# Performance work log

Hardware: AMD Instinct MI355X
Metric: run time of the kernel (lower is better)

## Reference

```python
import jax, jax.numpy as jnp
import numpy as np

N = 65536      # number of points
D = 3          # spatial dimension (init arg 'dimension')
C = 64         # feature channels
K = 16         # neighbors returned by faiss knn search
BLOCK = 512    # query block size for chunked brute-force distances
GRID = 128     # spatial_size


def setup_inputs() -> dict:
    key = jax.random.key(0)
    k1, k2 = jax.random.split(key)
    coords = jax.random.randint(k1, (N, D), 0, GRID, dtype=jnp.int32)
    features = jax.random.normal(k2, (N, C), dtype=jnp.float32)
    return {"coords": coords, "features": features}


def reference(coords, features):
    """Brute-force KNN over integer point coords (faiss-equivalent exact L2
    search), then sparse input-layer construction: for each point, gather the
    features of its K nearest neighbors and sum them (SCN InputLayer mode=3)."""
    cf = coords.astype(jnp.float32)                 # [N, D]
    db_sq = jnp.sum(cf * cf, axis=1)                # [N]

    n_blocks = N // BLOCK
    queries = cf.reshape(n_blocks, BLOCK, D)

    def step(_, q):                                 # q: [BLOCK, D]
        q_sq = jnp.sum(q * q, axis=1)               # [BLOCK]
        # squared L2 distances to all database points: [BLOCK, N]
        dist = q_sq[:, None] - 2.0 * (q @ cf.T) + db_sq[None, :]
        _, idx = jax.lax.top_k(-dist, K)            # [BLOCK, K] nearest indices
        nb = features[idx]                          # irregular gather [BLOCK, K, C]
        return None, jnp.sum(nb, axis=1)            # mode=3: sum duplicates/neighbors

    _, out = jax.lax.scan(step, None, queries)      # [n_blocks, BLOCK, C]
    return out.reshape(N, C)
```

## Files before the change

kernel.cpp:

```cpp
#include <hip/hip_runtime.h>


typedef unsigned int uint;
typedef unsigned short ushort;
typedef short short2v __attribute__((ext_vector_type(2)));

#define NPTS   65536
#define NCELL  32768
#define BBLK   256
#define BTPB   256

static __device__ inline short2v u2s(uint v) { union { uint u; short2v s; } c; c.u = v; return c.s; }
static __device__ inline uint s2u(short2v v) { union { uint u; short2v s; } c; c.s = v; return c.u; }

static __device__ inline int dot2acc(short2v a, short2v b, int c) {
#if __has_builtin(__builtin_amdgcn_sdot2)
    return __builtin_amdgcn_sdot2(a, b, c, false);
#else
    return (int)a.x * (int)b.x + (int)a.y * (int)b.y + c;
#endif
}

static __device__ __forceinline__ void gridbar(uint* bar, uint target) {
    __syncthreads();
    if (threadIdx.x == 0) {
        asm volatile("s_waitcnt vmcnt(0)" ::: "memory");
        __hip_atomic_fetch_add(bar, 1u, __ATOMIC_RELAXED, __HIP_MEMORY_SCOPE_AGENT);
        while (__hip_atomic_load(bar, __ATOMIC_RELAXED, __HIP_MEMORY_SCOPE_AGENT) < target)
            __builtin_amdgcn_s_sleep(4);
    }
    __syncthreads();
}

__global__ __launch_bounds__(BTPB) void build(const int* __restrict__ coords,
                                              uint* __restrict__ bar,
                                              uint* __restrict__ counts,
                                              uint* __restrict__ starts,
                                              uint* __restrict__ cursors,
                                              uint2* __restrict__ sorted) {
    __shared__ uint wsum[4];
    __shared__ uint rsum[4];
    int b = blockIdx.x, tid = threadIdx.x;
    int i = b * BTPB + tid;
    int lane = tid & 63, wv = tid >> 6;

    int x = coords[3 * i + 0], y = coords[3 * i + 1], z = coords[3 * i + 2];
    int cell = (x >> 2) | ((y >> 2) << 5) | ((z >> 2) << 10);
    atomicAdd(&counts[cell], 1u);
    gridbar(bar, BBLK);

    uint* bsums = (uint*)sorted;
    uint c = 0, excl = 0;
    if (b < 128) {
        int t2 = b * 256 + tid;
        c = __hip_atomic_load(&counts[t2], __ATOMIC_RELAXED, __HIP_MEMORY_SCOPE_AGENT);
        uint v = c;
#pragma unroll
        for (int off = 1; off < 64; off <<= 1) {
            uint u = __shfl_up(v, off, 64);
            if (lane >= off) v += u;
        }
        if (lane == 63) wsum[wv] = v;
        __syncthreads();
        uint woff = 0, btot = 0;
#pragma unroll
        for (int j = 0; j < 4; ++j) {
            uint w = wsum[j];
            woff += (j < wv) ? w : 0u;
            btot += w;
        }
        excl = woff + v - c;
        if (tid == 0)
            __hip_atomic_store(&bsums[b], btot, __ATOMIC_RELAXED, __HIP_MEMORY_SCOPE_AGENT);
    }
    gridbar(bar, 2 * BBLK);

    if (b < 128) {
        uint s = 0;
        if (tid < 128 && tid < b)
            s = __hip_atomic_load(&bsums[tid], __ATOMIC_RELAXED, __HIP_MEMORY_SCOPE_AGENT);
#pragma unroll
        for (int off = 32; off; off >>= 1) s += __shfl_xor(s, off, 64);
        if (lane == 0) rsum[wv] = s;
        __syncthreads();
        uint blockoff = rsum[0] + rsum[1] + rsum[2] + rsum[3];
        int t2 = b * 256 + tid;
        uint st = blockoff + excl;
        starts[t2] = st;
        __hip_atomic_store(&cursors[t2], st, __ATOMIC_RELAXED, __HIP_MEMORY_SCOPE_AGENT);
        if (t2 == NCELL - 1) starts[NCELL] = st + c;
    }
    gridbar(bar, 3 * BBLK);

    uint pos = atomicAdd(&cursors[cell], 1u);
    sorted[pos] = make_uint2((uint)(x | (y << 16)), (uint)(i | (z << 16)));
}

__global__ __launch_bounds__(256, 8) void knn_search(const uint* __restrict__ starts,
                                                     const uint2* __restrict__ sorted,
                                                     const float* __restrict__ feat,
                                                     float* __restrict__ out) {
    int blk  = (blockIdx.x & 7) * 256 + (blockIdx.x >> 3);
    int wave = threadIdx.x >> 6;
    int lane = threadIdx.x & 63;
    int qslot = lane & 7;
    int slice = lane >> 3;
    int qpos = blk * 32 + wave * 8 + qslot;

    uint2 me = sorted[qpos];
    uint qxy = me.x;
    uint qzp = me.y & 0xFFFF0000u;
    uint qidx = me.y & 0xFFFFu;
    int qx = (int)(me.x & 0xFFFFu);
    int qy = (int)(me.x >> 16);
    int qz = (int)(me.y >> 16);
    int cx = qx >> 2, cy = qy >> 2, cz = qz >> 2;

    uint k[16];
#pragma unroll
    for (int j = 0; j < 16; ++j) k[j] = 0xFFFFFFFFu;

    auto insert1 = [&](uint2 pt) {
        short2v A = u2s(pt.x) - u2s(qxy);
        short2v B = u2s(pt.y) - u2s(qzp);
        uint Bu = s2u(B);
        short2v Bm = u2s(Bu & 0xFFFF0000u);
        int d2 = dot2acc(A, A, dot2acc(Bm, Bm, 0));
        uint key = ((uint)d2 << 16) + (Bu & 0xFFFFu);
#pragma unroll
        for (int j = 15; j >= 1; --j)
            asm("v_med3_u32 %0, %1, %2, %3"
                : "=v"(k[j]) : "v"(k[j - 1]), "v"(k[j]), "v"(key));
        k[0] = min(k[0], key);
    };

    auto scan8 = [&](uint p0, uint p1) {
        for (uint p = p0 + (uint)slice; p < p1; p += 8u) insert1(sorted[p]);
    };

    auto merge_min = [&](int mask) {
        uint b[16];
#pragma unroll
        for (int j = 0; j < 16; ++j) b[j] = __shfl_xor(k[j], mask, 64);
#pragma unroll
        for (int j = 0; j < 16; ++j) k[j] = min(k[j], b[15 - j]);
    };
    auto clean = [&]() {
#pragma unroll
        for (int d = 8; d >= 1; d >>= 1) {
#pragma unroll
            for (int i = 0; i < 16; ++i) {
                if ((i & d) == 0) {
                    uint lo = min(k[i], k[i + d]);
                    uint hi = max(k[i], k[i + d]);
                    k[i] = lo;
                    k[i + d] = hi;
                }
            }
        }
    };
    auto merge = [&](int mask) { merge_min(mask); clean(); };
    auto merge_all = [&]() { merge(8); merge(16); merge(32); };

    int xa = min(max(cx - ((qx & 3) < 2 ? 2 : 1), 0), 28);
    int ya = min(max(cy - ((qy & 3) < 2 ? 2 : 1), 0), 28);
    int za = min(max(cz - ((qz & 3) < 2 ? 2 : 1), 0), 28);

    {
        int rbA = ((ya + (slice & 3)) << 5) | ((za + (slice >> 2)) << 10);
        int rbB = ((ya + (slice & 3)) << 5) | ((za + 2 + (slice >> 2)) << 10);
        uint pA = starts[rbA + xa], eA = starts[rbA + xa + 4];
        uint pB = starts[rbB + xa], eB = starts[rbB + xa + 4];
        while (__any((pA < eA) || (pB < eB))) {
            bool a0 = pA < eA, a1 = pA + 1 < eA;
            bool b0 = pB < eB, b1 = pB + 1 < eB;
            uint2 A0, A1, B0, B1;
            if (a0) A0 = sorted[pA];
            if (a1) A1 = sorted[pA + 1];
            if (b0) B0 = sorted[pB];
            if (b1) B1 = sorted[pB + 1];
            pA += (a0 ? 1u : 0u) + (a1 ? 1u : 0u);
            pB += (b0 ? 1u : 0u) + (b1 ? 1u : 0u);
            if (a0) insert1(A0);
            if (b0) insert1(B0);
            if (a1) insert1(A1);
            if (b1) insert1(B1);
        }
    }
    merge(8); merge(16); merge_min(32);
    uint mx = k[0];
#pragma unroll
    for (int j = 1; j < 16; ++j) mx = max(mx, k[j]);

    bool redo = (mx >> 16) >= 49u;
    if (__any(redo)) {
        clean();
        if (redo || slice != 0) {
#pragma unroll
            for (int j = 0; j < 16; ++j) k[j] = 0xFFFFFFFFu;
        }
        if (redo) {
            int xl = max(cx - 2, 0), xh = min(cx + 2, 31);
            int yl = max(cy - 2, 0), yh = min(cy + 2, 31);
            int zl = max(cz - 2, 0), zh = min(cz + 2, 31);
            for (int z = zl; z <= zh; ++z)
                for (int y = yl; y <= yh; ++y) {
                    int rb = (y << 5) | (z << 10);
                    scan8(starts[rb + xl], starts[rb + xh + 1]);
                }
        }
        merge_all();
        for (int r = 3; r < 32; ++r) {
            uint b = (uint)(4 * r - 3);
            bool active = (k[15] >> 16) >= b * b;
            if (!__any(active)) break;
            if (slice != 0) {
#pragma unroll
                for (int j = 0; j < 16; ++j) k[j] = 0xFFFFFFFFu;
            }
            if (active) {
                int z0 = cz - r < 0 ? 0 : cz - r;
                int z1 = cz + r > 31 ? 31 : cz + r;
                for (int z = z0; z <= z1; ++z) {
                    bool zface = (z == cz - r) || (z == cz + r);
                    int y0 = cy - r < 0 ? 0 : cy - r;
                    int y1 = cy + r > 31 ? 31 : cy + r;
                    for (int y = y0; y <= y1; ++y) {
                        bool face = zface || (y == cy - r) || (y == cy + r);
                        int rb = (y << 5) | (z << 10);
                        if (face) {
                            int x0 = cx - r < 0 ? 0 : cx - r;
                            int x1 = cx + r > 31 ? 31 : cx + r;
                            scan8(starts[rb + x0], starts[rb + x1 + 1]);
                        } else {
                            int xL = cx - r;
                            if (xL >= 0) scan8(starts[rb + xL], starts[rb + xL + 1]);
                            int xR = cx + r;
                            if (xR <= 31) scan8(starts[rb + xR], starts[rb + xR + 1]);
                        }
                    }
                }
            }
            merge_all();
        }
    }

    uint ki[16];
#pragma unroll
    for (int j = 0; j < 16; ++j) ki[j] = k[j] & 0xFFFFu;

    int ch = lane & 15;
    int qg = lane >> 4;
#pragma unroll
    for (int p = 0; p < 2; ++p) {
        int qs = p * 4 + qg;
        uint qorig = __shfl(qidx, qs, 64);
        float4 acc = make_float4(0.f, 0.f, 0.f, 0.f);
#pragma unroll
        for (int j = 0; j < 16; ++j) {
            uint nj = __shfl(ki[j], qs, 64);
            float4 v = reinterpret_cast<const float4*>(feat)[nj * 16u + (uint)ch];
            acc.x += v.x; acc.y += v.y; acc.z += v.z; acc.w += v.w;
        }
        reinterpret_cast<float4*>(out)[qorig * 16u + (uint)ch] = acc;
    }
}

extern "C" void kernel_launch(void* const* d_in, const int* in_sizes, int n_in,
                              void* d_out, int out_size, void* d_ws, size_t ws_size,
                              hipStream_t stream) {
    const int*   coords = (const int*)d_in[0];
    const float* feat   = (const float*)d_in[1];
    float*       out    = (float*)d_out;

    uint* W = (uint*)d_ws;
    uint*  bar     = W;
    uint*  counts  = W + 8;
    uint*  starts  = W + 32776;
    uint*  cursors = W + 65548;
    uint2* sorted  = (uint2*)(W + 98316);

    hipMemsetAsync(W, 0, (8 + NCELL) * sizeof(uint), stream);
    build<<<BBLK, BTPB, 0, stream>>>(coords, bar, counts, starts, cursors, sorted);
    knn_search<<<2048, 256, 0, stream>>>(starts, sorted, feat, out);
}
```

Measured before the change: 75.19 us.

## Split grid-barrier build kernel into count, chunked-scan and scatter kernels

```diff
diff --git a/kernel.cpp b/kernel.cpp
--- a/kernel.cpp
+++ b/kernel.cpp
@@ -7,8 +7,6 @@
 
 #define NPTS   65536
 #define NCELL  32768
-#define BBLK   256
-#define BTPB   256
 
 static __device__ inline short2v u2s(uint v) { union { uint u; short2v s; } c; c.u = v; return c.s; }
 static __device__ inline uint s2u(short2v v) { union { uint u; short2v s; } c; c.s = v; return c.u; }
@@ -21,82 +19,57 @@
 #endif
 }
 
-static __device__ __forceinline__ void gridbar(uint* bar, uint target) {
-    __syncthreads();
-    if (threadIdx.x == 0) {
-        asm volatile("s_waitcnt vmcnt(0)" ::: "memory");
-        __hip_atomic_fetch_add(bar, 1u, __ATOMIC_RELAXED, __HIP_MEMORY_SCOPE_AGENT);
-        while (__hip_atomic_load(bar, __ATOMIC_RELAXED, __HIP_MEMORY_SCOPE_AGENT) < target)
-            __builtin_amdgcn_s_sleep(4);
-    }
-    __syncthreads();
-}
-
-__global__ __launch_bounds__(BTPB) void build(const int* __restrict__ coords,
-                                              uint* __restrict__ bar,
-                                              uint* __restrict__ counts,
-                                              uint* __restrict__ starts,
-                                              uint* __restrict__ cursors,
-                                              uint2* __restrict__ sorted) {
-    __shared__ uint wsum[4];
-    __shared__ uint rsum[4];
-    int b = blockIdx.x, tid = threadIdx.x;
-    int i = b * BTPB + tid;
-    int lane = tid & 63, wv = tid >> 6;
-
+__global__ __launch_bounds__(256) void cell_count(const int* __restrict__ coords,
+                                                  uint* __restrict__ counts) {
+    int i = blockIdx.x * 256 + threadIdx.x;
     int x = coords[3 * i + 0], y = coords[3 * i + 1], z = coords[3 * i + 2];
     int cell = (x >> 2) | ((y >> 2) << 5) | ((z >> 2) << 10);
     atomicAdd(&counts[cell], 1u);
-    gridbar(bar, BBLK);
-
-    uint* bsums = (uint*)sorted;
-    uint c = 0, excl = 0;
-    if (b < 128) {
-        int t2 = b * 256 + tid;
-        c = __hip_atomic_load(&counts[t2], __ATOMIC_RELAXED, __HIP_MEMORY_SCOPE_AGENT);
-        uint v = c;
-#pragma unroll
-        for (int off = 1; off < 64; off <<= 1) {
-            uint u = __shfl_up(v, off, 64);
-            if (lane >= off) v += u;
-        }
-        if (lane == 63) wsum[wv] = v;
-        __syncthreads();
-        uint woff = 0, btot = 0;
-#pragma unroll
-        for (int j = 0; j < 4; ++j) {
-            uint w = wsum[j];
-            woff += (j < wv) ? w : 0u;
-            btot += w;
-        }
-        excl = woff + v - c;
-        if (tid == 0)
-            __hip_atomic_store(&bsums[b], btot, __ATOMIC_RELAXED, __HIP_MEMORY_SCOPE_AGENT);
-    }
-    gridbar(bar, 2 * BBLK);
-
-    if (b < 128) {
-        uint s = 0;
-        if (tid < 128 && tid < b)
-            s = __hip_atomic_load(&bsums[tid], __ATOMIC_RELAXED, __HIP_MEMORY_SCOPE_AGENT);
-#pragma unroll
-        for (int off = 32; off; off >>= 1) s += __shfl_xor(s, off, 64);
-        if (lane == 0) rsum[wv] = s;
-        __syncthreads();
-        uint blockoff = rsum[0] + rsum[1] + rsum[2] + rsum[3];
-        int t2 = b * 256 + tid;
-        uint st = blockoff + excl;
-        starts[t2] = st;
-        __hip_atomic_store(&cursors[t2], st, __ATOMIC_RELAXED, __HIP_MEMORY_SCOPE_AGENT);
-        if (t2 == NCELL - 1) starts[NCELL] = st + c;
-    }
-    gridbar(bar, 3 * BBLK);
-
+}
+
+__global__ __launch_bounds__(256) void scan_chunk(const uint* __restrict__ counts,
+                                                  uint* __restrict__ gcur,
+                                                  uint* __restrict__ starts,
+                                                  uint* __restrict__ ends,
+                                                  uint* __restrict__ cursors) {
+    __shared__ uint wsum[4];
+    __shared__ uint sbase;
+    int tid = threadIdx.x;
+    int lane = tid & 63, wv = tid >> 6;
+    int cell = blockIdx.x * 256 + tid;
+    uint c = counts[cell];
+    uint v = c;
+#pragma unroll
+    for (int off = 1; off < 64; off <<= 1) {
+        uint u = __shfl_up(v, off, 64);
+        if (lane >= off) v += u;
+    }
+    if (lane == 63) wsum[wv] = v;
+    __syncthreads();
+    if (tid == 0)
+        sbase = atomicAdd(gcur, wsum[0] + wsum[1] + wsum[2] + wsum[3]);
+    __syncthreads();
+    uint woff = 0;
+#pragma unroll
+    for (int j = 0; j < 4; ++j) woff += (j < wv) ? wsum[j] : 0u;
+    uint st = sbase + woff + v - c;
+    starts[cell]  = st;
+    ends[cell]    = st + c;
+    cursors[cell] = st;
+}
+
+__global__ __launch_bounds__(256) void cell_scatter(const int* __restrict__ coords,
+                                                    uint* __restrict__ cursors,
+                                                    uint2* __restrict__ sorted) {
+    int i = blockIdx.x * 256 + threadIdx.x;
+    int x = coords[3 * i + 0], y = coords[3 * i + 1], z = coords[3 * i + 2];
+    int cell = (x >> 2) | ((y >> 2) << 5) | ((z >> 2) << 10);
     uint pos = atomicAdd(&cursors[cell], 1u);
     sorted[pos] = make_uint2((uint)(x | (y << 16)), (uint)(i | (z << 16)));
 }
 
 __global__ __launch_bounds__(256, 8) void knn_search(const uint* __restrict__ starts,
+                                                     const uint* __restrict__ ends,
                                                      const uint2* __restrict__ sorted,
                                                      const float* __restrict__ feat,
                                                      float* __restrict__ out) {
@@ -169,8 +142,8 @@
     {
         int rbA = ((ya + (slice & 3)) << 5) | ((za + (slice >> 2)) << 10);
         int rbB = ((ya + (slice & 3)) << 5) | ((za + 2 + (slice >> 2)) << 10);
-        uint pA = starts[rbA + xa], eA = starts[rbA + xa + 4];
-        uint pB = starts[rbB + xa], eB = starts[rbB + xa + 4];
+        uint pA = starts[rbA + xa], eA = ends[rbA + xa + 3];
+        uint pB = starts[rbB + xa], eB = ends[rbB + xa + 3];
         while (__any((pA < eA) || (pB < eB))) {
             bool a0 = pA < eA, a1 = pA + 1 < eA;
             bool b0 = pB < eB, b1 = pB + 1 < eB;
@@ -206,7 +179,7 @@
             for (int z = zl; z <= zh; ++z)
                 for (int y = yl; y <= yh; ++y) {
                     int rb = (y << 5) | (z << 10);
-                    scan8(starts[rb + xl], starts[rb + xh + 1]);
+                    scan8(starts[rb + xl], ends[rb + xh]);
                 }
         }
         merge_all();
@@ -231,12 +204,12 @@
                         if (face) {
                             int x0 = cx - r < 0 ? 0 : cx - r;
                             int x1 = cx + r > 31 ? 31 : cx + r;
-                            scan8(starts[rb + x0], starts[rb + x1 + 1]);
+                            scan8(starts[rb + x0], ends[rb + x1]);
                         } else {
                             int xL = cx - r;
-                            if (xL >= 0) scan8(starts[rb + xL], starts[rb + xL + 1]);
+                            if (xL >= 0) scan8(starts[rb + xL], ends[rb + xL]);
                             int xR = cx + r;
-                            if (xR <= 31) scan8(starts[rb + xR], starts[rb + xR + 1]);
+                            if (xR <= 31) scan8(starts[rb + xR], ends[rb + xR]);
                         }
                     }
                 }
@@ -274,13 +247,16 @@
     float*       out    = (float*)d_out;
 
     uint* W = (uint*)d_ws;
-    uint*  bar     = W;
+    uint*  gcur    = W;
     uint*  counts  = W + 8;
     uint*  starts  = W + 32776;
-    uint*  cursors = W + 65548;
-    uint2* sorted  = (uint2*)(W + 98316);
+    uint*  ends    = W + 65544;
+    uint*  cursors = W + 98312;
+    uint2* sorted  = (uint2*)(W + 131080);
 
     hipMemsetAsync(W, 0, (8 + NCELL) * sizeof(uint), stream);
-    build<<<BBLK, BTPB, 0, stream>>>(coords, bar, counts, starts, cursors, sorted);
-    knn_search<<<2048, 256, 0, stream>>>(starts, sorted, feat, out);
-}
+    cell_count<<<NPTS / 256, 256, 0, stream>>>(coords, counts);
+    scan_chunk<<<NCELL / 256, 256, 0, stream>>>(counts, gcur, starts, ends, cursors);
+    cell_scatter<<<NPTS / 256, 256, 0, stream>>>(coords, cursors, sorted);
+    knn_search<<<2048, 256, 0, stream>>>(starts, ends, sorted, feat, out);
+}
```

After: 61.50 us. 18.2% less time.
